# Kernel optimization log

Hardware: AMD Instinct MI355X
Metric: run time of the kernel (lower is better)

The kernel has to match this reference:

```python
import jax, jax.numpy as jnp
import numpy as np

# SOM hyperparameters (match init_kwargs)
M, N = 64, 64
NODES = M * N
FEATS = 256
BATCH = 1024
LR = 0.5
RADIUS_FACTOR = 1.1
TOTAL_ITER = 100000
SIGMA = max(M, N) * RADIUS_FACTOR


def setup_inputs() -> dict:
    key = jax.random.key(0)
    k1, k2 = jax.random.split(key)
    x = jax.random.uniform(k1, (BATCH, FEATS), dtype=jnp.float32)
    map_w = jax.random.uniform(k2, (NODES, FEATS), dtype=jnp.float32)
    return {"x": x, "map_w": map_w, "iteration": 0}


def _grid_locs():
    ii, jj = jnp.meshgrid(jnp.arange(M), jnp.arange(N), indexing='ij')
    return jnp.stack([ii.ravel(), jj.ravel()], axis=1)  # (NODES, 2) int32


def reference(x, map_w, iteration):
    B = x.shape[0]
    # ---- feedforward: squared distances (B, NODES) via GEMM expansion,
    # avoiding the (B, NODES, FEATS) broadcast the TF code materializes.
    x2 = jnp.sum(x * x, axis=1, keepdims=True)          # (B, 1)
    w2 = jnp.sum(map_w * map_w, axis=1)                  # (NODES,)
    sqd = x2 + w2[None, :] - 2.0 * (x @ map_w.T)         # (B, NODES)
    bmu_indices = jnp.argmin(sqd, axis=1)                # (B,)

    # ---- backprop: neighborhood-weighted codebook update
    locs = _grid_locs()                                  # (NODES, 2)
    bmu_locs = locs[bmu_indices]                         # (B, 2)
    # grid distance^2 between every node and each sample's BMU: (B, NODES)
    d2 = jnp.sum((locs[None, :, :] - bmu_locs[:, None, :]) ** 2, axis=2).astype(jnp.float32)

    lambda_g = TOTAL_ITER / SIGMA
    decay = jnp.exp(jnp.float32(-float(iteration) / lambda_g))
    radius = SIGMA * decay + 1e-6
    lr = LR * decay

    impact = jnp.exp(-d2 / (2.0 * radius * radius))
    in_radius = (jnp.sqrt(d2) <= radius).astype(jnp.float32)
    lr_op = impact * in_radius * lr                      # (B, NODES)

    # weight_update[n,d] = sum_b lr_op[b,n] * (x[b,d] - map_w[n,d])
    # computed without the (B, NODES, FEATS) intermediate:
    upd = (jnp.einsum('bn,bd->nd', lr_op, x) - lr_op.sum(axis=0)[:, None] * map_w) / B
    new_map = map_w + upd
    return new_map, bmu_indices
```

## Files before the change

### kernel.cpp

```cpp
#include <hip/hip_runtime.h>
#include <math.h>

#define NODES 4096
#define FEATS 256
#define BATCH 1024
#define LR_C 0.5f
#define SIGMA_C 70.4f

typedef _Float16 f16x8 __attribute__((ext_vector_type(8)));
typedef float floatx4 __attribute__((ext_vector_type(4)));

__device__ __forceinline__ void get_params(int it, float& lr, float& r2, float& i2r2) {
    float decay = __expf(-(float)it * (SIGMA_C / 100000.0f));
    float radius = SIGMA_C * decay + 1e-6f;
    lr = LR_C * decay;
    r2 = radius * radius;
    i2r2 = 1.0f / (2.0f * r2);
}

__global__ __launch_bounds__(256) void k_prep_w(const float* __restrict__ Wm,
                                                _Float16* __restrict__ Wh, float* __restrict__ w2) {
    int row = blockIdx.x * 4 + (threadIdx.x >> 6);
    int lane = threadIdx.x & 63;
    float4 v = *(const float4*)&Wm[(size_t)row * FEATS + lane * 4];
    union { _Float16 h[4]; float2 f2; } u;
    u.h[0] = (_Float16)v.x; u.h[1] = (_Float16)v.y; u.h[2] = (_Float16)v.z; u.h[3] = (_Float16)v.w;
    *(float2*)&Wh[(size_t)row * FEATS + lane * 4] = u.f2;
    float s = v.x * v.x + v.y * v.y + v.z * v.z + v.w * v.w;
#pragma unroll
    for (int off = 32; off > 0; off >>= 1) s += __shfl_down(s, off, 64);
    if (lane == 0) w2[row] = s;
}

__global__ __launch_bounds__(256) void k_prep_x(const float* __restrict__ X,
                                                _Float16* __restrict__ Xh, _Float16* __restrict__ XT) {
    __shared__ _Float16 T[64][72];
    const int b0 = blockIdx.x * 64;
    const int d0 = blockIdx.y * 64;
    const int t = threadIdx.x;
    {
        const int bl = t >> 2, dq = (t & 3) * 16;
        union { _Float16 h[16]; float4 q[2]; } u;
#pragma unroll
        for (int c = 0; c < 4; ++c) {
            float4 v = *(const float4*)&X[(size_t)(b0 + bl) * FEATS + d0 + dq + c * 4];
            u.h[c * 4 + 0] = (_Float16)v.x; u.h[c * 4 + 1] = (_Float16)v.y;
            u.h[c * 4 + 2] = (_Float16)v.z; u.h[c * 4 + 3] = (_Float16)v.w;
        }
        *(float4*)&Xh[(size_t)(b0 + bl) * FEATS + d0 + dq] = u.q[0];
        *(float4*)&Xh[(size_t)(b0 + bl) * FEATS + d0 + dq + 8] = u.q[1];
#pragma unroll
        for (int c = 0; c < 16; ++c) T[bl][dq + c] = u.h[c];
    }
    __syncthreads();
    {
        const int dl = t >> 2, bq = (t & 3) * 16;
        union { _Float16 h[16]; float4 q[2]; } u;
#pragma unroll
        for (int c = 0; c < 16; ++c) u.h[c] = T[bq + c][dl];
        *(float4*)&XT[(size_t)(d0 + dl) * BATCH + b0 + bq] = u.q[0];
        *(float4*)&XT[(size_t)(d0 + dl) * BATCH + b0 + bq + 8] = u.q[1];
    }
}

__global__ __launch_bounds__(256) void k_gemm1(const _Float16* __restrict__ Xh, const _Float16* __restrict__ Wh,
                                               const float* __restrict__ w2, _Float16* __restrict__ Sd) {
    __shared__ _Float16 As[64][40];
    __shared__ _Float16 Bs[64][40];
    const int n0 = blockIdx.x * 64;
    const int b0 = blockIdx.y * 64;
    const int t = threadIdx.x;
    const int wave = t >> 6, lane = t & 63;
    const int wm = wave & 1, wn = wave >> 1;
    const int lm = lane & 15, quad = lane >> 4;
    const int srow = t >> 2, skoff = (t & 3) * 8;
    floatx4 acc[2][2] = {};
    for (int k0 = 0; k0 < FEATS; k0 += 32) {
        *(float4*)&As[srow][skoff] = *(const float4*)&Xh[(size_t)(b0 + srow) * FEATS + k0 + skoff];
        *(float4*)&Bs[srow][skoff] = *(const float4*)&Wh[(size_t)(n0 + srow) * FEATS + k0 + skoff];
        __syncthreads();
        f16x8 af0 = *(f16x8*)&As[wm * 32 + lm][quad * 8];
        f16x8 af1 = *(f16x8*)&As[wm * 32 + 16 + lm][quad * 8];
        f16x8 bf0 = *(f16x8*)&Bs[wn * 32 + lm][quad * 8];
        f16x8 bf1 = *(f16x8*)&Bs[wn * 32 + 16 + lm][quad * 8];
        acc[0][0] = __builtin_amdgcn_mfma_f32_16x16x32_f16(af0, bf0, acc[0][0], 0, 0, 0);
        acc[0][1] = __builtin_amdgcn_mfma_f32_16x16x32_f16(af0, bf1, acc[0][1], 0, 0, 0);
        acc[1][0] = __builtin_amdgcn_mfma_f32_16x16x32_f16(af1, bf0, acc[1][0], 0, 0, 0);
        acc[1][1] = __builtin_amdgcn_mfma_f32_16x16x32_f16(af1, bf1, acc[1][1], 0, 0, 0);
        __syncthreads();
    }
#pragma unroll
    for (int i = 0; i < 2; ++i)
#pragma unroll
        for (int j = 0; j < 2; ++j) {
            int col = n0 + wn * 32 + j * 16 + lm;
            float w2c = w2[col];
#pragma unroll
            for (int r = 0; r < 4; ++r) {
                int row = b0 + wm * 32 + i * 16 + quad * 4 + r;
                Sd[(size_t)row * NODES + col] = (_Float16)(w2c - 2.0f * acc[i][j][r]);
            }
        }
}

__global__ __launch_bounds__(256) void k_argmin(const _Float16* __restrict__ Sd, const float* __restrict__ X,
                                                const float* __restrict__ Wm, const float* __restrict__ w2,
                                                int* __restrict__ bmu, float* __restrict__ out1) {
    __shared__ float sv[256];
    __shared__ int si[256];
    __shared__ float red[256];
    __shared__ int cand[128];
    __shared__ int cnt;
    const int b = blockIdx.x;
    const int t = threadIdx.x;
    const _Float16* row = Sd + (size_t)b * NODES;
    float v[16];
#pragma unroll
    for (int j = 0; j < 2; ++j) {
        f16x8 h = *(const f16x8*)&row[j * 2048 + t * 8];
#pragma unroll
        for (int u = 0; u < 8; ++u) v[j * 8 + u] = (float)h[u];
    }
    float best = INFINITY;
    int bidx = 0;
#pragma unroll
    for (int j = 0; j < 2; ++j)
#pragma unroll
        for (int u = 0; u < 8; ++u) {
            int n = j * 2048 + t * 8 + u;
            if (v[j * 8 + u] < best) { best = v[j * 8 + u]; bidx = n; }
        }
    sv[t] = best; si[t] = bidx;
    if (t == 0) cnt = 0;
    __syncthreads();
    for (int g = 128; g > 0; g >>= 1) {
        if (t < g) {
            float v2 = sv[t + g]; int i2 = si[t + g];
            if (v2 < sv[t] || (v2 == sv[t] && i2 < si[t])) { sv[t] = v2; si[t] = i2; }
        }
        __syncthreads();
    }
    const float thr = sv[0] + 0.4f;
#pragma unroll
    for (int j = 0; j < 2; ++j)
#pragma unroll
        for (int u = 0; u < 8; ++u) {
            if (v[j * 8 + u] <= thr) {
                int p = atomicAdd(&cnt, 1);
                if (p < 128) cand[p] = j * 2048 + t * 8 + u;
            }
        }
    __syncthreads();
    const int C = cnt < 128 ? cnt : 128;
    const float xv = X[(size_t)b * FEATS + t];
    float bestv = INFINITY;
    int besti = NODES;
    for (int c = 0; c < C; ++c) {
        int n = cand[c];
        red[t] = xv * Wm[(size_t)n * FEATS + t];
        __syncthreads();
        for (int g = 128; g > 0; g >>= 1) {
            if (t < g) red[t] += red[t + g];
            __syncthreads();
        }
        if (t == 0) {
            float ex = w2[n] - 2.0f * red[0];
            if (ex < bestv || (ex == bestv && n < besti)) { bestv = ex; besti = n; }
        }
        __syncthreads();
    }
    if (t == 0) { bmu[b] = besti; out1[b] = (float)besti; }
}

__global__ __launch_bounds__(256) void k_lrop(const int* __restrict__ bmu, const int* __restrict__ itp,
                                              _Float16* __restrict__ lrT, float* __restrict__ Svec) {
    __shared__ int bmu_s[1024];
    __shared__ float texp[64];
    __shared__ float red4[4];
    const int t = threadIdx.x;
#pragma unroll
    for (int j = 0; j < 4; ++j) bmu_s[t + j * 256] = bmu[t + j * 256];
    float lr, r2, i2r2;
    get_params(itp[0], lr, r2, i2r2);
    if (t < 64) texp[t] = __expf(-(float)(t * t) * i2r2);
    __syncthreads();
    const int n = blockIdx.x * 2 + (t >> 7);
    const int b0 = (t & 127) * 8;
    const int ni = n >> 6, nj = n & 63;
    float s = 0.0f;
    union { _Float16 h[8]; float4 q; } u;
#pragma unroll
    for (int c = 0; c < 8; ++c) {
        int m = bmu_s[b0 + c];
        int di = ni - (m >> 6); di = di < 0 ? -di : di;
        int dj = nj - (m & 63); dj = dj < 0 ? -dj : dj;
        int d2 = di * di + dj * dj;
        float val = ((float)d2 <= r2) ? lr * texp[di] * texp[dj] : 0.0f;
        u.h[c] = (_Float16)val;
        s += val;
    }
    *(float4*)&lrT[(size_t)n * BATCH + b0] = u.q;
    const int lane = t & 63, wave = t >> 6;
#pragma unroll
    for (int off = 32; off > 0; off >>= 1) s += __shfl_down(s, off, 64);
    if (lane == 0) red4[wave] = s;
    __syncthreads();
    if (t < 2) Svec[blockIdx.x * 2 + t] = red4[2 * t] + red4[2 * t + 1];
}

__global__ __launch_bounds__(256) void k_gemm2(const _Float16* __restrict__ lrT, const _Float16* __restrict__ XT,
                                               float* __restrict__ P) {
    __shared__ _Float16 As[64][40];
    __shared__ _Float16 Bs[64][40];
    const int d0 = blockIdx.x * 64;
    const int n0 = blockIdx.y * 64;
    const int z = blockIdx.z;
    const int t = threadIdx.x;
    const int wave = t >> 6, lane = t & 63;
    const int wm = wave & 1, wn = wave >> 1;
    const int lm = lane & 15, quad = lane >> 4;
    const int srow = t >> 2, skoff = (t & 3) * 8;
    const size_t kbase = (size_t)z * 512;
    floatx4 acc[2][2] = {};
    for (int k0 = 0; k0 < 512; k0 += 32) {
        *(float4*)&As[srow][skoff] = *(const float4*)&lrT[(size_t)(n0 + srow) * BATCH + kbase + k0 + skoff];
        *(float4*)&Bs[srow][skoff] = *(const float4*)&XT[(size_t)(d0 + srow) * BATCH + kbase + k0 + skoff];
        __syncthreads();
        f16x8 af0 = *(f16x8*)&As[wm * 32 + lm][quad * 8];
        f16x8 af1 = *(f16x8*)&As[wm * 32 + 16 + lm][quad * 8];
        f16x8 bf0 = *(f16x8*)&Bs[wn * 32 + lm][quad * 8];
        f16x8 bf1 = *(f16x8*)&Bs[wn * 32 + 16 + lm][quad * 8];
        acc[0][0] = __builtin_amdgcn_mfma_f32_16x16x32_f16(af0, bf0, acc[0][0], 0, 0, 0);
        acc[0][1] = __builtin_amdgcn_mfma_f32_16x16x32_f16(af0, bf1, acc[0][1], 0, 0, 0);
        acc[1][0] = __builtin_amdgcn_mfma_f32_16x16x32_f16(af1, bf0, acc[1][0], 0, 0, 0);
        acc[1][1] = __builtin_amdgcn_mfma_f32_16x16x32_f16(af1, bf1, acc[1][1], 0, 0, 0);
        __syncthreads();
    }
    float* Pz = P + (size_t)z * NODES * FEATS;
#pragma unroll
    for (int i = 0; i < 2; ++i)
#pragma unroll
        for (int j = 0; j < 2; ++j) {
            int col = d0 + wn * 32 + j * 16 + lm;
#pragma unroll
            for (int r = 0; r < 4; ++r) {
                int row = n0 + wm * 32 + i * 16 + quad * 4 + r;
                Pz[(size_t)row * FEATS + col] = acc[i][j][r];
            }
        }
}

__global__ __launch_bounds__(256) void k_combine(const float* __restrict__ Wm, const float* __restrict__ P,
                                                 const float* __restrict__ Svec, float* __restrict__ out0) {
    const int g = blockIdx.x * 256 + threadIdx.x;
    const int n = g >> 6;
    const float invB = 1.0f / (float)BATCH;
    float4 w4 = *(const float4*)&Wm[(size_t)g * 4];
    float4 p0 = *(const float4*)&P[(size_t)g * 4];
    float4 p1 = *(const float4*)&P[(size_t)NODES * FEATS + (size_t)g * 4];
    float c = 1.0f - Svec[n] * invB;
    float4 o;
    o.x = w4.x * c + (p0.x + p1.x) * invB;
    o.y = w4.y * c + (p0.y + p1.y) * invB;
    o.z = w4.z * c + (p0.z + p1.z) * invB;
    o.w = w4.w * c + (p0.w + p1.w) * invB;
    *(float4*)&out0[(size_t)g * 4] = o;
}

extern "C" void kernel_launch(void* const* d_in, const int* in_sizes, int n_in,
                              void* d_out, int out_size, void* d_ws, size_t ws_size,
                              hipStream_t stream) {
    const float* X = (const float*)d_in[0];
    const float* Wm = (const float*)d_in[1];
    const int* itp = (const int*)d_in[2];
    float* out = (float*)d_out;

    char* ws = (char*)d_ws;
    float* w2       = (float*)(ws + 0);
    _Float16* Xh    = (_Float16*)(ws + 16384);
    _Float16* XT    = (_Float16*)(ws + 540672);
    _Float16* Wh    = (_Float16*)(ws + 1064960);
    int* bmu        = (int*)(ws + 3162112);
    float* Svec     = (float*)(ws + 3166208);
    _Float16* Sd    = (_Float16*)(ws + 3182592);
    _Float16* lrT   = (_Float16*)(ws + 3182592);
    float* P        = (float*)(ws + 11571200);

    k_prep_w<<<1024, 256, 0, stream>>>(Wm, Wh, w2);
    k_prep_x<<<dim3(16, 4), 256, 0, stream>>>(X, Xh, XT);
    k_gemm1<<<dim3(64, 16), 256, 0, stream>>>(Xh, Wh, w2, Sd);
    k_argmin<<<1024, 256, 0, stream>>>(Sd, X, Wm, w2, bmu, out + (size_t)NODES * FEATS);
    k_lrop<<<2048, 256, 0, stream>>>(bmu, itp, lrT, Svec);
    k_gemm2<<<dim3(4, 64, 2), 256, 0, stream>>>(lrT, XT, P);
    k_combine<<<1024, 256, 0, stream>>>(Wm, P, Svec, out);
}
```

Measured before the change: 110.4 us.

## Fuse pipeline into persistent cooperative megakernel with grid syncs and fused row-min

Replaces the seven separate kernel launches with one persistent cooperative kernel of 512 blocks. The phases are separated by grid-wide syncs, and a per-phase launch fallback is kept if the cooperative launch fails. The first GEMM now computes each row's minimum in its epilogue with packed 64-bit atomicMin, so the argmin phase only filters candidates and no longer needs a block-wide reduction. The exact candidate re-check is spread across waves, and the lr_op phase handles more nodes per block. This aims to cut launch overhead and the reduction work, at the cost of grid-sync latency and fewer resident blocks for the GEMM phases.

```diff
diff --git a/kernel.cpp b/kernel.cpp
--- a/kernel.cpp
+++ b/kernel.cpp
@@ -1,11 +1,15 @@
 #include <hip/hip_runtime.h>
+#include <hip/hip_cooperative_groups.h>
 #include <math.h>
+
+namespace cg = cooperative_groups;
 
 #define NODES 4096
 #define FEATS 256
 #define BATCH 1024
 #define LR_C 0.5f
 #define SIGMA_C 70.4f
+#define GRID 512
 
 typedef _Float16 f16x8 __attribute__((ext_vector_type(8)));
 typedef float floatx4 __attribute__((ext_vector_type(4)));
@@ -18,253 +22,265 @@
     i2r2 = 1.0f / (2.0f * r2);
 }
 
-__global__ __launch_bounds__(256) void k_prep_w(const float* __restrict__ Wm,
-                                                _Float16* __restrict__ Wh, float* __restrict__ w2) {
-    int row = blockIdx.x * 4 + (threadIdx.x >> 6);
-    int lane = threadIdx.x & 63;
-    float4 v = *(const float4*)&Wm[(size_t)row * FEATS + lane * 4];
-    union { _Float16 h[4]; float2 f2; } u;
-    u.h[0] = (_Float16)v.x; u.h[1] = (_Float16)v.y; u.h[2] = (_Float16)v.z; u.h[3] = (_Float16)v.w;
-    *(float2*)&Wh[(size_t)row * FEATS + lane * 4] = u.f2;
-    float s = v.x * v.x + v.y * v.y + v.z * v.z + v.w * v.w;
-#pragma unroll
-    for (int off = 32; off > 0; off >>= 1) s += __shfl_down(s, off, 64);
-    if (lane == 0) w2[row] = s;
-}
-
-__global__ __launch_bounds__(256) void k_prep_x(const float* __restrict__ X,
-                                                _Float16* __restrict__ Xh, _Float16* __restrict__ XT) {
-    __shared__ _Float16 T[64][72];
-    const int b0 = blockIdx.x * 64;
-    const int d0 = blockIdx.y * 64;
-    const int t = threadIdx.x;
-    {
-        const int bl = t >> 2, dq = (t & 3) * 16;
-        union { _Float16 h[16]; float4 q[2]; } u;
-#pragma unroll
-        for (int c = 0; c < 4; ++c) {
-            float4 v = *(const float4*)&X[(size_t)(b0 + bl) * FEATS + d0 + dq + c * 4];
-            u.h[c * 4 + 0] = (_Float16)v.x; u.h[c * 4 + 1] = (_Float16)v.y;
-            u.h[c * 4 + 2] = (_Float16)v.z; u.h[c * 4 + 3] = (_Float16)v.w;
-        }
-        *(float4*)&Xh[(size_t)(b0 + bl) * FEATS + d0 + dq] = u.q[0];
-        *(float4*)&Xh[(size_t)(b0 + bl) * FEATS + d0 + dq + 8] = u.q[1];
-#pragma unroll
-        for (int c = 0; c < 16; ++c) T[bl][dq + c] = u.h[c];
-    }
-    __syncthreads();
-    {
-        const int dl = t >> 2, bq = (t & 3) * 16;
-        union { _Float16 h[16]; float4 q[2]; } u;
-#pragma unroll
-        for (int c = 0; c < 16; ++c) u.h[c] = T[bq + c][dl];
-        *(float4*)&XT[(size_t)(d0 + dl) * BATCH + b0 + bq] = u.q[0];
-        *(float4*)&XT[(size_t)(d0 + dl) * BATCH + b0 + bq + 8] = u.q[1];
-    }
-}
-
-__global__ __launch_bounds__(256) void k_gemm1(const _Float16* __restrict__ Xh, const _Float16* __restrict__ Wh,
-                                               const float* __restrict__ w2, _Float16* __restrict__ Sd) {
+__device__ __forceinline__ unsigned fkey(float f) {
+    unsigned u = __float_as_uint(f);
+    return (u & 0x80000000u) ? ~u : (u | 0x80000000u);
+}
+__device__ __forceinline__ float funkey(unsigned k) {
+    unsigned u = (k & 0x80000000u) ? (k & 0x7fffffffu) : ~k;
+    return __uint_as_float(u);
+}
+__device__ __forceinline__ unsigned long long shfl_xor_u64(unsigned long long v, int mask) {
+    unsigned lo = (unsigned)v, hi = (unsigned)(v >> 32);
+    lo = __shfl_xor(lo, mask, 64);
+    hi = __shfl_xor(hi, mask, 64);
+    return ((unsigned long long)hi << 32) | lo;
+}
+
+__global__ __launch_bounds__(256, 2) void mega(
+    int ph0, int ph1, int coop,
+    const float* __restrict__ X, const float* __restrict__ Wm, const int* __restrict__ itp,
+    float* __restrict__ out0, float* __restrict__ out1,
+    float* __restrict__ w2, _Float16* __restrict__ Xh, _Float16* __restrict__ XT,
+    _Float16* __restrict__ Wh, int* __restrict__ bmu, float* __restrict__ Svec,
+    _Float16* __restrict__ SdLr, float* __restrict__ P, unsigned long long* __restrict__ gmin)
+{
     __shared__ _Float16 As[64][40];
     __shared__ _Float16 Bs[64][40];
-    const int n0 = blockIdx.x * 64;
-    const int b0 = blockIdx.y * 64;
-    const int t = threadIdx.x;
-    const int wave = t >> 6, lane = t & 63;
-    const int wm = wave & 1, wn = wave >> 1;
-    const int lm = lane & 15, quad = lane >> 4;
-    const int srow = t >> 2, skoff = (t & 3) * 8;
-    floatx4 acc[2][2] = {};
-    for (int k0 = 0; k0 < FEATS; k0 += 32) {
-        *(float4*)&As[srow][skoff] = *(const float4*)&Xh[(size_t)(b0 + srow) * FEATS + k0 + skoff];
-        *(float4*)&Bs[srow][skoff] = *(const float4*)&Wh[(size_t)(n0 + srow) * FEATS + k0 + skoff];
-        __syncthreads();
-        f16x8 af0 = *(f16x8*)&As[wm * 32 + lm][quad * 8];
-        f16x8 af1 = *(f16x8*)&As[wm * 32 + 16 + lm][quad * 8];
-        f16x8 bf0 = *(f16x8*)&Bs[wn * 32 + lm][quad * 8];
-        f16x8 bf1 = *(f16x8*)&Bs[wn * 32 + 16 + lm][quad * 8];
-        acc[0][0] = __builtin_amdgcn_mfma_f32_16x16x32_f16(af0, bf0, acc[0][0], 0, 0, 0);
-        acc[0][1] = __builtin_amdgcn_mfma_f32_16x16x32_f16(af0, bf1, acc[0][1], 0, 0, 0);
-        acc[1][0] = __builtin_amdgcn_mfma_f32_16x16x32_f16(af1, bf0, acc[1][0], 0, 0, 0);
-        acc[1][1] = __builtin_amdgcn_mfma_f32_16x16x32_f16(af1, bf1, acc[1][1], 0, 0, 0);
-        __syncthreads();
-    }
-#pragma unroll
-    for (int i = 0; i < 2; ++i)
-#pragma unroll
-        for (int j = 0; j < 2; ++j) {
-            int col = n0 + wn * 32 + j * 16 + lm;
-            float w2c = w2[col];
-#pragma unroll
-            for (int r = 0; r < 4; ++r) {
-                int row = b0 + wm * 32 + i * 16 + quad * 4 + r;
-                Sd[(size_t)row * NODES + col] = (_Float16)(w2c - 2.0f * acc[i][j][r]);
-            }
-        }
-}
-
-__global__ __launch_bounds__(256) void k_argmin(const _Float16* __restrict__ Sd, const float* __restrict__ X,
-                                                const float* __restrict__ Wm, const float* __restrict__ w2,
-                                                int* __restrict__ bmu, float* __restrict__ out1) {
-    __shared__ float sv[256];
-    __shared__ int si[256];
-    __shared__ float red[256];
+    __shared__ _Float16 T[64][72];
+    __shared__ unsigned long long rowmin[64][2];
     __shared__ int cand[128];
     __shared__ int cnt;
-    const int b = blockIdx.x;
-    const int t = threadIdx.x;
-    const _Float16* row = Sd + (size_t)b * NODES;
-    float v[16];
-#pragma unroll
-    for (int j = 0; j < 2; ++j) {
-        f16x8 h = *(const f16x8*)&row[j * 2048 + t * 8];
-#pragma unroll
-        for (int u = 0; u < 8; ++u) v[j * 8 + u] = (float)h[u];
-    }
-    float best = INFINITY;
-    int bidx = 0;
-#pragma unroll
-    for (int j = 0; j < 2; ++j)
-#pragma unroll
-        for (int u = 0; u < 8; ++u) {
-            int n = j * 2048 + t * 8 + u;
-            if (v[j * 8 + u] < best) { best = v[j * 8 + u]; bidx = n; }
-        }
-    sv[t] = best; si[t] = bidx;
-    if (t == 0) cnt = 0;
-    __syncthreads();
-    for (int g = 128; g > 0; g >>= 1) {
-        if (t < g) {
-            float v2 = sv[t + g]; int i2 = si[t + g];
-            if (v2 < sv[t] || (v2 == sv[t] && i2 < si[t])) { sv[t] = v2; si[t] = i2; }
-        }
-        __syncthreads();
-    }
-    const float thr = sv[0] + 0.4f;
-#pragma unroll
-    for (int j = 0; j < 2; ++j)
-#pragma unroll
-        for (int u = 0; u < 8; ++u) {
-            if (v[j * 8 + u] <= thr) {
-                int p = atomicAdd(&cnt, 1);
-                if (p < 128) cand[p] = j * 2048 + t * 8 + u;
-            }
-        }
-    __syncthreads();
-    const int C = cnt < 128 ? cnt : 128;
-    const float xv = X[(size_t)b * FEATS + t];
-    float bestv = INFINITY;
-    int besti = NODES;
-    for (int c = 0; c < C; ++c) {
-        int n = cand[c];
-        red[t] = xv * Wm[(size_t)n * FEATS + t];
-        __syncthreads();
-        for (int g = 128; g > 0; g >>= 1) {
-            if (t < g) red[t] += red[t + g];
-            __syncthreads();
-        }
-        if (t == 0) {
-            float ex = w2[n] - 2.0f * red[0];
-            if (ex < bestv || (ex == bestv && n < besti)) { bestv = ex; besti = n; }
-        }
-        __syncthreads();
-    }
-    if (t == 0) { bmu[b] = besti; out1[b] = (float)besti; }
-}
-
-__global__ __launch_bounds__(256) void k_lrop(const int* __restrict__ bmu, const int* __restrict__ itp,
-                                              _Float16* __restrict__ lrT, float* __restrict__ Svec) {
+    __shared__ unsigned long long wbest[4];
     __shared__ int bmu_s[1024];
     __shared__ float texp[64];
-    __shared__ float red4[4];
+
     const int t = threadIdx.x;
-#pragma unroll
-    for (int j = 0; j < 4; ++j) bmu_s[t + j * 256] = bmu[t + j * 256];
-    float lr, r2, i2r2;
-    get_params(itp[0], lr, r2, i2r2);
-    if (t < 64) texp[t] = __expf(-(float)(t * t) * i2r2);
-    __syncthreads();
-    const int n = blockIdx.x * 2 + (t >> 7);
-    const int b0 = (t & 127) * 8;
-    const int ni = n >> 6, nj = n & 63;
-    float s = 0.0f;
-    union { _Float16 h[8]; float4 q; } u;
-#pragma unroll
-    for (int c = 0; c < 8; ++c) {
-        int m = bmu_s[b0 + c];
-        int di = ni - (m >> 6); di = di < 0 ? -di : di;
-        int dj = nj - (m & 63); dj = dj < 0 ? -dj : dj;
-        int d2 = di * di + dj * dj;
-        float val = ((float)d2 <= r2) ? lr * texp[di] * texp[dj] : 0.0f;
-        u.h[c] = (_Float16)val;
-        s += val;
+    const int blk = blockIdx.x;
+    const int wave = t >> 6, lane = t & 63;
+
+    for (int ph = ph0; ph < ph1; ++ph) {
+        if (ph == 0) {
+#pragma unroll
+            for (int rr = 0; rr < 2; ++rr) {
+                int row = blk * 8 + wave * 2 + rr;
+                float4 v = *(const float4*)&Wm[(size_t)row * FEATS + lane * 4];
+                union { _Float16 h[4]; float2 f2; } u;
+                u.h[0] = (_Float16)v.x; u.h[1] = (_Float16)v.y;
+                u.h[2] = (_Float16)v.z; u.h[3] = (_Float16)v.w;
+                *(float2*)&Wh[(size_t)row * FEATS + lane * 4] = u.f2;
+                float s = v.x * v.x + v.y * v.y + v.z * v.z + v.w * v.w;
+#pragma unroll
+                for (int off = 32; off > 0; off >>= 1) s += __shfl_down(s, off, 64);
+                if (lane == 0) w2[row] = s;
+            }
+            if (blk < 4) gmin[blk * 256 + t] = 0xFFFFFFFFFFFFFFFFULL;
+            if (blk < 64) {
+                const int b0 = (blk & 15) * 64, d0 = (blk >> 4) * 64;
+                {
+                    const int bl = t >> 2, dq = (t & 3) * 16;
+                    union { _Float16 h[16]; float4 q[2]; } u;
+#pragma unroll
+                    for (int c = 0; c < 4; ++c) {
+                        float4 v = *(const float4*)&X[(size_t)(b0 + bl) * FEATS + d0 + dq + c * 4];
+                        u.h[c * 4 + 0] = (_Float16)v.x; u.h[c * 4 + 1] = (_Float16)v.y;
+                        u.h[c * 4 + 2] = (_Float16)v.z; u.h[c * 4 + 3] = (_Float16)v.w;
+                    }
+                    *(float4*)&Xh[(size_t)(b0 + bl) * FEATS + d0 + dq] = u.q[0];
+                    *(float4*)&Xh[(size_t)(b0 + bl) * FEATS + d0 + dq + 8] = u.q[1];
+#pragma unroll
+                    for (int c = 0; c < 16; ++c) T[bl][dq + c] = u.h[c];
+                }
+                __syncthreads();
+                {
+                    const int dl = t >> 2, bq = (t & 3) * 16;
+                    union { _Float16 h[16]; float4 q[2]; } u;
+#pragma unroll
+                    for (int c = 0; c < 16; ++c) u.h[c] = T[bq + c][dl];
+                    *(float4*)&XT[(size_t)(d0 + dl) * BATCH + b0 + bq] = u.q[0];
+                    *(float4*)&XT[(size_t)(d0 + dl) * BATCH + b0 + bq + 8] = u.q[1];
+                }
+            }
+        } else if (ph == 1) {
+            const int wm = wave & 1, wn = wave >> 1;
+            const int lm = lane & 15, quad = lane >> 4;
+            const int srow = t >> 2, skoff = (t & 3) * 8;
+            for (int tile = blk; tile < 1024; tile += GRID) {
+                const int n0 = (tile & 63) * 64;
+                const int b0 = (tile >> 6) * 64;
+                floatx4 acc[2][2] = {};
+                for (int k0 = 0; k0 < FEATS; k0 += 32) {
+                    *(float4*)&As[srow][skoff] = *(const float4*)&Xh[(size_t)(b0 + srow) * FEATS + k0 + skoff];
+                    *(float4*)&Bs[srow][skoff] = *(const float4*)&Wh[(size_t)(n0 + srow) * FEATS + k0 + skoff];
+                    __syncthreads();
+                    f16x8 af0 = *(f16x8*)&As[wm * 32 + lm][quad * 8];
+                    f16x8 af1 = *(f16x8*)&As[wm * 32 + 16 + lm][quad * 8];
+                    f16x8 bf0 = *(f16x8*)&Bs[wn * 32 + lm][quad * 8];
+                    f16x8 bf1 = *(f16x8*)&Bs[wn * 32 + 16 + lm][quad * 8];
+                    acc[0][0] = __builtin_amdgcn_mfma_f32_16x16x32_f16(af0, bf0, acc[0][0], 0, 0, 0);
+                    acc[0][1] = __builtin_amdgcn_mfma_f32_16x16x32_f16(af0, bf1, acc[0][1], 0, 0, 0);
+                    acc[1][0] = __builtin_amdgcn_mfma_f32_16x16x32_f16(af1, bf0, acc[1][0], 0, 0, 0);
+                    acc[1][1] = __builtin_amdgcn_mfma_f32_16x16x32_f16(af1, bf1, acc[1][1], 0, 0, 0);
+                    __syncthreads();
+                }
+                const int col0 = n0 + wn * 32 + lm, col1 = col0 + 16;
+                const float w20 = w2[col0], w21 = w2[col1];
+#pragma unroll
+                for (int i = 0; i < 2; ++i) {
+#pragma unroll
+                    for (int r = 0; r < 4; ++r) {
+                        int row = b0 + wm * 32 + i * 16 + quad * 4 + r;
+                        float va = w20 - 2.0f * acc[i][0][r];
+                        float vb = w21 - 2.0f * acc[i][1][r];
+                        SdLr[(size_t)row * NODES + col0] = (_Float16)va;
+                        SdLr[(size_t)row * NODES + col1] = (_Float16)vb;
+                        unsigned long long ka = ((unsigned long long)fkey(va) << 32) | (unsigned)col0;
+                        unsigned long long kb = ((unsigned long long)fkey(vb) << 32) | (unsigned)col1;
+                        unsigned long long m = ka < kb ? ka : kb;
+#pragma unroll
+                        for (int mk = 1; mk < 16; mk <<= 1) {
+                            unsigned long long o = shfl_xor_u64(m, mk);
+                            if (o < m) m = o;
+                        }
+                        if (lm == 0) rowmin[wm * 32 + i * 16 + quad * 4 + r][wn] = m;
+                    }
+                }
+                __syncthreads();
+                if (t < 64) {
+                    unsigned long long v = rowmin[t][0];
+                    if (rowmin[t][1] < v) v = rowmin[t][1];
+                    atomicMin(&gmin[b0 + t], v);
+                }
+                __syncthreads();
+            }
+        } else if (ph == 2) {
+            for (int b = blk; b < BATCH; b += GRID) {
+                if (t == 0) cnt = 0;
+                if (t < 4) wbest[t] = 0xFFFFFFFFFFFFFFFFULL;
+                __syncthreads();
+                const _Float16* row = SdLr + (size_t)b * NODES;
+                const float thr = funkey((unsigned)(gmin[b] >> 32)) + 0.4f;
+#pragma unroll
+                for (int j = 0; j < 2; ++j) {
+                    f16x8 h = *(const f16x8*)&row[j * 2048 + t * 8];
+#pragma unroll
+                    for (int u = 0; u < 8; ++u) {
+                        if ((float)h[u] <= thr) {
+                            int p = atomicAdd(&cnt, 1);
+                            if (p < 128) cand[p] = j * 2048 + t * 8 + u;
+                        }
+                    }
+                }
+                __syncthreads();
+                const int C = cnt < 128 ? cnt : 128;
+                float4 xv = *(const float4*)&X[(size_t)b * FEATS + lane * 4];
+                unsigned long long best = 0xFFFFFFFFFFFFFFFFULL;
+                for (int c = wave; c < C; c += 4) {
+                    int n = cand[c];
+                    float4 wv = *(const float4*)&Wm[(size_t)n * FEATS + lane * 4];
+                    float d = xv.x * wv.x + xv.y * wv.y + xv.z * wv.z + xv.w * wv.w;
+#pragma unroll
+                    for (int off = 32; off > 0; off >>= 1) d += __shfl_down(d, off, 64);
+                    if (lane == 0) {
+                        float ex = w2[n] - 2.0f * d;
+                        unsigned long long k = ((unsigned long long)fkey(ex) << 32) | (unsigned)n;
+                        if (k < best) best = k;
+                    }
+                }
+                if (lane == 0) wbest[wave] = best;
+                __syncthreads();
+                if (t == 0) {
+                    unsigned long long bb = wbest[0];
+#pragma unroll
+                    for (int w2i = 1; w2i < 4; ++w2i) if (wbest[w2i] < bb) bb = wbest[w2i];
+                    int idx = (int)(bb & 0xFFFFFFFFULL);
+                    bmu[b] = idx;
+                    out1[b] = (float)idx;
+                }
+                __syncthreads();
+            }
+        } else if (ph == 3) {
+#pragma unroll
+            for (int j = 0; j < 4; ++j) bmu_s[t + j * 256] = bmu[t + j * 256];
+            float lr, r2, i2r2;
+            get_params(itp[0], lr, r2, i2r2);
+            if (t < 64) texp[t] = __expf(-(float)(t * t) * i2r2);
+            __syncthreads();
+            const int n = blk * 8 + (t >> 5);
+            const int b0 = (t & 31) * 32;
+            const int ni = n >> 6, nj = n & 63;
+            float s = 0.0f;
+            union { _Float16 h[32]; float4 q[4]; } u;
+#pragma unroll
+            for (int c = 0; c < 32; ++c) {
+                int m = bmu_s[b0 + c];
+                int di = ni - (m >> 6); di = di < 0 ? -di : di;
+                int dj = nj - (m & 63); dj = dj < 0 ? -dj : dj;
+                int d2 = di * di + dj * dj;
+                float val = ((float)d2 <= r2) ? lr * texp[di] * texp[dj] : 0.0f;
+                u.h[c] = (_Float16)val;
+                s += val;
+            }
+#pragma unroll
+            for (int q4 = 0; q4 < 4; ++q4)
+                *(float4*)&SdLr[(size_t)n * BATCH + b0 + q4 * 8] = u.q[q4];
+#pragma unroll
+            for (int off = 16; off > 0; off >>= 1) s += __shfl_down(s, off, 32);
+            if ((t & 31) == 0) Svec[n] = s;
+        } else if (ph == 4) {
+            const int z = blk >> 8, rest = blk & 255;
+            const int d0 = (rest & 3) * 64, n0 = (rest >> 2) * 64;
+            const int wm = wave & 1, wn = wave >> 1;
+            const int lm = lane & 15, quad = lane >> 4;
+            const int srow = t >> 2, skoff = (t & 3) * 8;
+            const size_t kbase = (size_t)z * 512;
+            floatx4 acc[2][2] = {};
+            for (int k0 = 0; k0 < 512; k0 += 32) {
+                *(float4*)&As[srow][skoff] = *(const float4*)&SdLr[(size_t)(n0 + srow) * BATCH + kbase + k0 + skoff];
+                *(float4*)&Bs[srow][skoff] = *(const float4*)&XT[(size_t)(d0 + srow) * BATCH + kbase + k0 + skoff];
+                __syncthreads();
+                f16x8 af0 = *(f16x8*)&As[wm * 32 + lm][quad * 8];
+                f16x8 af1 = *(f16x8*)&As[wm * 32 + 16 + lm][quad * 8];
+                f16x8 bf0 = *(f16x8*)&Bs[wn * 32 + lm][quad * 8];
+                f16x8 bf1 = *(f16x8*)&Bs[wn * 32 + 16 + lm][quad * 8];
+                acc[0][0] = __builtin_amdgcn_mfma_f32_16x16x32_f16(af0, bf0, acc[0][0], 0, 0, 0);
+                acc[0][1] = __builtin_amdgcn_mfma_f32_16x16x32_f16(af0, bf1, acc[0][1], 0, 0, 0);
+                acc[1][0] = __builtin_amdgcn_mfma_f32_16x16x32_f16(af1, bf0, acc[1][0], 0, 0, 0);
+                acc[1][1] = __builtin_amdgcn_mfma_f32_16x16x32_f16(af1, bf1, acc[1][1], 0, 0, 0);
+                __syncthreads();
+            }
+            float* Pz = P + (size_t)z * NODES * FEATS;
+#pragma unroll
+            for (int i = 0; i < 2; ++i)
+#pragma unroll
+                for (int j = 0; j < 2; ++j) {
+                    int col = d0 + wn * 32 + j * 16 + lm;
+#pragma unroll
+                    for (int r = 0; r < 4; ++r) {
+                        int row = n0 + wm * 32 + i * 16 + quad * 4 + r;
+                        Pz[(size_t)row * FEATS + col] = acc[i][j][r];
+                    }
+                }
+        } else {
+            const float invB = 1.0f / (float)BATCH;
+#pragma unroll
+            for (int it2 = 0; it2 < 2; ++it2) {
+                int g = it2 * (GRID * 256) + blk * 256 + t;
+                int n = g >> 6;
+                float4 w4 = *(const float4*)&Wm[(size_t)g * 4];
+                float4 p0 = *(const float4*)&P[(size_t)g * 4];
+                float4 p1 = *(const float4*)&P[(size_t)NODES * FEATS + (size_t)g * 4];
+                float c = 1.0f - Svec[n] * invB;
+                float4 o;
+                o.x = w4.x * c + (p0.x + p1.x) * invB;
+                o.y = w4.y * c + (p0.y + p1.y) * invB;
+                o.z = w4.z * c + (p0.z + p1.z) * invB;
+                o.w = w4.w * c + (p0.w + p1.w) * invB;
+                *(float4*)&out0[(size_t)g * 4] = o;
+            }
+        }
+        if (coop && ph + 1 < ph1) cg::this_grid().sync();
     }
-    *(float4*)&lrT[(size_t)n * BATCH + b0] = u.q;
-    const int lane = t & 63, wave = t >> 6;
-#pragma unroll
-    for (int off = 32; off > 0; off >>= 1) s += __shfl_down(s, off, 64);
-    if (lane == 0) red4[wave] = s;
-    __syncthreads();
-    if (t < 2) Svec[blockIdx.x * 2 + t] = red4[2 * t] + red4[2 * t + 1];
-}
-
-__global__ __launch_bounds__(256) void k_gemm2(const _Float16* __restrict__ lrT, const _Float16* __restrict__ XT,
-                                               float* __restrict__ P) {
-    __shared__ _Float16 As[64][40];
-    __shared__ _Float16 Bs[64][40];
-    const int d0 = blockIdx.x * 64;
-    const int n0 = blockIdx.y * 64;
-    const int z = blockIdx.z;
-    const int t = threadIdx.x;
-    const int wave = t >> 6, lane = t & 63;
-    const int wm = wave & 1, wn = wave >> 1;
-    const int lm = lane & 15, quad = lane >> 4;
-    const int srow = t >> 2, skoff = (t & 3) * 8;
-    const size_t kbase = (size_t)z * 512;
-    floatx4 acc[2][2] = {};
-    for (int k0 = 0; k0 < 512; k0 += 32) {
-        *(float4*)&As[srow][skoff] = *(const float4*)&lrT[(size_t)(n0 + srow) * BATCH + kbase + k0 + skoff];
-        *(float4*)&Bs[srow][skoff] = *(const float4*)&XT[(size_t)(d0 + srow) * BATCH + kbase + k0 + skoff];
-        __syncthreads();
-        f16x8 af0 = *(f16x8*)&As[wm * 32 + lm][quad * 8];
-        f16x8 af1 = *(f16x8*)&As[wm * 32 + 16 + lm][quad * 8];
-        f16x8 bf0 = *(f16x8*)&Bs[wn * 32 + lm][quad * 8];
-        f16x8 bf1 = *(f16x8*)&Bs[wn * 32 + 16 + lm][quad * 8];
-        acc[0][0] = __builtin_amdgcn_mfma_f32_16x16x32_f16(af0, bf0, acc[0][0], 0, 0, 0);
-        acc[0][1] = __builtin_amdgcn_mfma_f32_16x16x32_f16(af0, bf1, acc[0][1], 0, 0, 0);
-        acc[1][0] = __builtin_amdgcn_mfma_f32_16x16x32_f16(af1, bf0, acc[1][0], 0, 0, 0);
-        acc[1][1] = __builtin_amdgcn_mfma_f32_16x16x32_f16(af1, bf1, acc[1][1], 0, 0, 0);
-        __syncthreads();
-    }
-    float* Pz = P + (size_t)z * NODES * FEATS;
-#pragma unroll
-    for (int i = 0; i < 2; ++i)
-#pragma unroll
-        for (int j = 0; j < 2; ++j) {
-            int col = d0 + wn * 32 + j * 16 + lm;
-#pragma unroll
-            for (int r = 0; r < 4; ++r) {
-                int row = n0 + wm * 32 + i * 16 + quad * 4 + r;
-                Pz[(size_t)row * FEATS + col] = acc[i][j][r];
-            }
-        }
-}
-
-__global__ __launch_bounds__(256) void k_combine(const float* __restrict__ Wm, const float* __restrict__ P,
-                                                 const float* __restrict__ Svec, float* __restrict__ out0) {
-    const int g = blockIdx.x * 256 + threadIdx.x;
-    const int n = g >> 6;
-    const float invB = 1.0f / (float)BATCH;
-    float4 w4 = *(const float4*)&Wm[(size_t)g * 4];
-    float4 p0 = *(const float4*)&P[(size_t)g * 4];
-    float4 p1 = *(const float4*)&P[(size_t)NODES * FEATS + (size_t)g * 4];
-    float c = 1.0f - Svec[n] * invB;
-    float4 o;
-    o.x = w4.x * c + (p0.x + p1.x) * invB;
-    o.y = w4.y * c + (p0.y + p1.y) * invB;
-    o.z = w4.z * c + (p0.z + p1.z) * invB;
-    o.w = w4.w * c + (p0.w + p1.w) * invB;
-    *(float4*)&out0[(size_t)g * 4] = o;
 }
 
 extern "C" void kernel_launch(void* const* d_in, const int* in_sizes, int n_in,
@@ -273,7 +289,8 @@
     const float* X = (const float*)d_in[0];
     const float* Wm = (const float*)d_in[1];
     const int* itp = (const int*)d_in[2];
-    float* out = (float*)d_out;
+    float* out0 = (float*)d_out;
+    float* out1 = out0 + (size_t)NODES * FEATS;
 
     char* ws = (char*)d_ws;
     float* w2       = (float*)(ws + 0);
@@ -282,15 +299,18 @@
     _Float16* Wh    = (_Float16*)(ws + 1064960);
     int* bmu        = (int*)(ws + 3162112);
     float* Svec     = (float*)(ws + 3166208);
-    _Float16* Sd    = (_Float16*)(ws + 3182592);
-    _Float16* lrT   = (_Float16*)(ws + 3182592);
+    _Float16* SdLr  = (_Float16*)(ws + 3182592);
     float* P        = (float*)(ws + 11571200);
-
-    k_prep_w<<<1024, 256, 0, stream>>>(Wm, Wh, w2);
-    k_prep_x<<<dim3(16, 4), 256, 0, stream>>>(X, Xh, XT);
-    k_gemm1<<<dim3(64, 16), 256, 0, stream>>>(Xh, Wh, w2, Sd);
-    k_argmin<<<1024, 256, 0, stream>>>(Sd, X, Wm, w2, bmu, out + (size_t)NODES * FEATS);
-    k_lrop<<<2048, 256, 0, stream>>>(bmu, itp, lrT, Svec);
-    k_gemm2<<<dim3(4, 64, 2), 256, 0, stream>>>(lrT, XT, P);
-    k_combine<<<1024, 256, 0, stream>>>(Wm, P, Svec, out);
-}
+    unsigned long long* gmin = (unsigned long long*)(ws + 19959808);
+
+    int ph0 = 0, ph1 = 6, coop = 1;
+    void* args[] = { &ph0, &ph1, &coop, &X, &Wm, &itp, &out0, &out1,
+                     &w2, &Xh, &XT, &Wh, &bmu, &Svec, &SdLr, &P, &gmin };
+    hipError_t e = hipLaunchCooperativeKernel((const void*)mega, dim3(GRID), dim3(256), args, 0, stream);
+    if (e != hipSuccess) {
+        (void)hipGetLastError();
+        for (int p = 0; p < 6; ++p)
+            mega<<<GRID, 256, 0, stream>>>(p, p + 1, 0, X, Wm, itp, out0, out1,
+                                           w2, Xh, XT, Wh, bmu, Svec, SdLr, P, gmin);
+    }
+}
```

Result: slower. 433.6 us (+292.9%).
